# Kernel optimization log

Hardware: AMD Instinct MI355X
Metric: run time of the kernel (lower is better)

## Reference

```python
import jax, jax.numpy as jnp
import numpy as np

B, NL, NP = 8, 256, 16384
DL, DP = 10, 4          # ligand / protein atom-type vocab sizes (one-hot prefix)
L_BIND, L_MREG = 1.0, 0.1
DELTA, EPS, A_C, B_C = 0.01, 1.0, 1.0, 1.0
BOX = 30.0              # Angstrom box for coordinates


def setup_inputs() -> dict:
    key = jax.random.key(0)
    ks = jax.random.split(key, 10)
    return {
        "predicted_noise": jax.random.normal(ks[0], (B, NL, 3), jnp.float32),
        "target_coords": jax.random.normal(ks[1], (B, NL, 3), jnp.float32),
        "scaffold_coords": jax.random.normal(ks[2], (B, NL, 3), jnp.float32),
        "target_coords2": jax.random.uniform(ks[3], (B, NL, 3), jnp.float32) * BOX,
        "target_features": jax.random.uniform(ks[4], (B, NL, DL), jnp.float32),
        "mask": jax.random.uniform(ks[5], (B, NL), jnp.float32),
        "protein_coords": jax.random.uniform(ks[6], (B, NP, 3), jnp.float32) * BOX,
        "protein_features": jax.random.uniform(ks[7], (B, NP, DP), jnp.float32),
        "lig_charge_table": jax.random.normal(ks[8], (DL,), jnp.float32) * 0.3,
        "prot_charge_table": jax.random.normal(ks[9], (DP,), jnp.float32) * 0.3,
    }


def _cdist(x, p):
    # x: [B, NL, 3], p: [B, NP, 3] -> [B, NL, NP] Euclidean distances
    x2 = jnp.sum(x * x, axis=-1)
    p2 = jnp.sum(p * p, axis=-1)
    d2 = x2[:, :, None] + p2[:, None, :] - 2.0 * jnp.einsum('bnd,bmd->bnm', x, p)
    return jnp.sqrt(jnp.maximum(d2, 0.0))


def _binding_energy(x0, prot, lig_feat, prot_feat, lig_tab, prot_tab):
    # atom charges from one-hot prefix of features (argmax lookup)
    ql = lig_tab[jnp.argmax(lig_feat[..., :DL], axis=-1)]    # [B, NL]
    qp = prot_tab[jnp.argmax(prot_feat[..., :DP], axis=-1)]  # [B, NP]
    d = _cdist(x0, prot) + DELTA                             # [B, NL, NP]
    inv = 1.0 / d
    inv6 = inv ** 6
    elec = jnp.sum(ql[:, :, None] * qp[:, None, :] * inv / EPS, axis=(1, 2))
    vdw = jnp.sum(A_C * inv6 * inv6 - B_C * inv6, axis=(1, 2))
    return elec + vdw  # [B]


def reference(predicted_noise, target_coords, scaffold_coords, target_coords2,
              target_features, mask, protein_coords, protein_features,
              lig_charge_table, prot_charge_table):
    msum = jnp.sum(mask)
    # masked denoising MSE
    mse = (predicted_noise - target_coords) ** 2
    loss_denoise = jnp.sum(mse * mask[..., None]) / msum
    # protein-guided binding energy, mean over batch
    loss_bind = jnp.mean(_binding_energy(target_coords2, protein_coords,
                                         target_features, protein_features,
                                         lig_charge_table, prot_charge_table))
    # mask regularization
    mask_diff = jnp.sum((scaffold_coords - target_coords) ** 2, axis=-1)
    loss_mreg = jnp.sum(mask_diff * mask) / msum
    return loss_denoise + L_BIND * loss_bind + L_MREG * loss_mreg
```

## Files before the change

### kernel.cpp

```cpp
#include <hip/hip_runtime.h>
#include <math.h>

#define B   8
#define NL  256
#define NP  16384
#define DL  10
#define DP  4

#define DELTA  0.01f

static __device__ __forceinline__ float fast_sqrtf(float x) {
#if __has_builtin(__builtin_amdgcn_sqrtf)
    return __builtin_amdgcn_sqrtf(x);
#else
    return sqrtf(x);
#endif
}
static __device__ __forceinline__ float fast_rcpf(float x) {
#if __has_builtin(__builtin_amdgcn_rcpf)
    return __builtin_amdgcn_rcpf(x);
#else
    return 1.0f / x;
#endif
}

#define NBIND 2048
#define NMSE  8

__global__ __launch_bounds__(256) void pair_mse_kernel(
    const float* __restrict__ prot_coords,
    const float* __restrict__ prot_feat,
    const float* __restrict__ tc2,
    const float* __restrict__ lig_feat,
    const float* __restrict__ lig_tab,
    const float* __restrict__ prot_tab,
    const float* __restrict__ pred_noise,
    const float* __restrict__ tgt_coords,
    const float* __restrict__ scaf_coords,
    const float* __restrict__ mask,
    double* __restrict__ partials)
{
    const int tid = threadIdx.x;
    const int blk = blockIdx.x;

    if (blk < NBIND) {
        const int lchunk = blk & 3;
        const int pchunk = (blk >> 2) & 63;
        const int b      = blk >> 8;

        __shared__ float4 slig[64];
        if (tid < 64) {
            const int li = b * NL + lchunk * 64 + tid;
            const float* f = lig_feat + (size_t)li * DL;
            float best = f[0]; float q = lig_tab[0];
            #pragma unroll
            for (int j = 1; j < DL; ++j) {
                float v = f[j];
                float t = lig_tab[j];
                if (v > best) { best = v; q = t; }
            }
            const float* c = tc2 + (size_t)li * 3;
            slig[tid] = make_float4(c[0], c[1], c[2], q);
        }

        const int m = b * NP + pchunk * 256 + tid;
        const float* pc = prot_coords + (size_t)m * 3;
        const float px = pc[0], py = pc[1], pz = pc[2];
        const float4 pf = reinterpret_cast<const float4*>(prot_feat)[m];
        float qb = pf.x, qp = prot_tab[0];
        { float t = prot_tab[1]; if (pf.y > qb) { qb = pf.y; qp = t; } }
        { float t = prot_tab[2]; if (pf.z > qb) { qb = pf.z; qp = t; } }
        { float t = prot_tab[3]; if (pf.w > qb) { qb = pf.w; qp = t; } }

        __syncthreads();

        float eacc = 0.0f, vacc = 0.0f;
        #pragma unroll 8
        for (int j = 0; j < 64; ++j) {
            const float4 l = slig[j];
            float dx = l.x - px;
            float dy = l.y - py;
            float dz = l.z - pz;
            float d2 = fmaf(dx, dx, fmaf(dy, dy, dz * dz));
            float d  = fast_sqrtf(d2) + DELTA;
            float inv  = fast_rcpf(d);
            float inv2 = inv * inv;
            float inv6 = inv2 * inv2 * inv2;
            eacc = fmaf(l.w, inv, eacc);
            vacc = fmaf(inv6, inv6 - 1.0f, vacc);
        }
        double e = (double)(qp * eacc);
        double v = (double)vacc;

        #pragma unroll
        for (int off = 32; off > 0; off >>= 1) {
            e += __shfl_down(e, off, 64);
            v += __shfl_down(v, off, 64);
        }
        __shared__ double se[4], sv[4];
        const int lane = tid & 63, w = tid >> 6;
        if (lane == 0) { se[w] = e; sv[w] = v; }
        __syncthreads();
        if (tid == 0) {
            partials[2 * blk]     = se[0] + se[1] + se[2] + se[3];
            partials[2 * blk + 1] = sv[0] + sv[1] + sv[2] + sv[3];
        }
    } else {
        const int idx = blk - NBIND;
        const int i   = idx * 256 + tid;
        float mk = mask[i];
        float a0 = pred_noise[3*i+0] - tgt_coords[3*i+0];
        float a1 = pred_noise[3*i+1] - tgt_coords[3*i+1];
        float a2 = pred_noise[3*i+2] - tgt_coords[3*i+2];
        double de = (double)mk * ((double)a0*a0 + (double)a1*a1 + (double)a2*a2);
        float s0 = scaf_coords[3*i+0] - tgt_coords[3*i+0];
        float s1 = scaf_coords[3*i+1] - tgt_coords[3*i+1];
        float s2 = scaf_coords[3*i+2] - tgt_coords[3*i+2];
        double mr = (double)mk * ((double)s0*s0 + (double)s1*s1 + (double)s2*s2);
        double ms = (double)mk;

        #pragma unroll
        for (int off = 32; off > 0; off >>= 1) {
            de += __shfl_down(de, off, 64);
            mr += __shfl_down(mr, off, 64);
            ms += __shfl_down(ms, off, 64);
        }
        __shared__ double s[4][3];
        const int lane = tid & 63, w = tid >> 6;
        if (lane == 0) { s[w][0] = de; s[w][1] = mr; s[w][2] = ms; }
        __syncthreads();
        if (tid == 0) {
            partials[2*NBIND + idx*3 + 0] = s[0][0]+s[1][0]+s[2][0]+s[3][0];
            partials[2*NBIND + idx*3 + 1] = s[0][1]+s[1][1]+s[2][1]+s[3][1];
            partials[2*NBIND + idx*3 + 2] = s[0][2]+s[1][2]+s[2][2]+s[3][2];
        }
    }
}

__global__ __launch_bounds__(256) void finalize_kernel(
    const double* __restrict__ partials,
    float* __restrict__ out)
{
    const int tid = threadIdx.x;
    double el = 0.0, vd = 0.0;
    for (int i = tid; i < NBIND; i += 256) {
        el += partials[2*i];
        vd += partials[2*i + 1];
    }
    double de = 0.0, mr = 0.0, ms = 0.0;
    if (tid < NMSE) {
        de = partials[2*NBIND + tid*3 + 0];
        mr = partials[2*NBIND + tid*3 + 1];
        ms = partials[2*NBIND + tid*3 + 2];
    }
    #pragma unroll
    for (int off = 32; off > 0; off >>= 1) {
        el += __shfl_down(el, off, 64);
        vd += __shfl_down(vd, off, 64);
        de += __shfl_down(de, off, 64);
        mr += __shfl_down(mr, off, 64);
        ms += __shfl_down(ms, off, 64);
    }
    __shared__ double s[4][5];
    const int lane = tid & 63, w = tid >> 6;
    if (lane == 0) { s[w][0]=el; s[w][1]=vd; s[w][2]=de; s[w][3]=mr; s[w][4]=ms; }
    __syncthreads();
    if (tid == 0) {
        el = s[0][0]+s[1][0]+s[2][0]+s[3][0];
        vd = s[0][1]+s[1][1]+s[2][1]+s[3][1];
        de = s[0][2]+s[1][2]+s[2][2]+s[3][2];
        mr = s[0][3]+s[1][3]+s[2][3]+s[3][3];
        ms = s[0][4]+s[1][4]+s[2][4]+s[3][4];
        double loss_bind = (el + vd) / (double)B;
        double loss = de / ms + loss_bind + 0.1 * (mr / ms);
        out[0] = (float)loss;
    }
}

extern "C" void kernel_launch(void* const* d_in, const int* in_sizes, int n_in,
                              void* d_out, int out_size, void* d_ws, size_t ws_size,
                              hipStream_t stream)
{
    const float* pred_noise  = (const float*)d_in[0];
    const float* tgt_coords  = (const float*)d_in[1];
    const float* scaf_coords = (const float*)d_in[2];
    const float* tc2         = (const float*)d_in[3];
    const float* lig_feat    = (const float*)d_in[4];
    const float* mask        = (const float*)d_in[5];
    const float* prot_coords = (const float*)d_in[6];
    const float* prot_feat   = (const float*)d_in[7];
    const float* lig_tab     = (const float*)d_in[8];
    const float* prot_tab    = (const float*)d_in[9];
    float* out = (float*)d_out;

    double* partials = (double*)d_ws;

    pair_mse_kernel<<<NBIND + NMSE, 256, 0, stream>>>(
        prot_coords, prot_feat, tc2, lig_feat, lig_tab, prot_tab,
        pred_noise, tgt_coords, scaf_coords, mask, partials);
    finalize_kernel<<<1, 256, 0, stream>>>(partials, out);
}
```

Baseline: 94.97 us.

## Fuse finalize into main kernel via last-block atomic counter and pack pair math

Removes the separate finalize kernel launch. Each block bumps an atomic counter after writing its partials, and the last block to arrive does the final reduction and writes the loss. A memset of the counter is added before the launch. The inner pair loop is also restructured to handle two ligand atoms at once using float2 vectors from SoA shared arrays, aiming for packed FP32 math. The risks are the added memset operation and relying on correct memory ordering between blocks.

```diff
diff --git a/kernel.cpp b/kernel.cpp
--- a/kernel.cpp
+++ b/kernel.cpp
@@ -8,6 +8,12 @@
 #define DP  4
 
 #define DELTA  0.01f
+
+#define NBIND 2048
+#define NMSE  8
+#define NBLK  (NBIND + NMSE)
+
+typedef float v2f __attribute__((ext_vector_type(2)));
 
 static __device__ __forceinline__ float fast_sqrtf(float x) {
 #if __has_builtin(__builtin_amdgcn_sqrtf)
@@ -24,10 +30,7 @@
 #endif
 }
 
-#define NBIND 2048
-#define NMSE  8
-
-__global__ __launch_bounds__(256) void pair_mse_kernel(
+__global__ __launch_bounds__(256) void fused_kernel(
     const float* __restrict__ prot_coords,
     const float* __restrict__ prot_feat,
     const float* __restrict__ tc2,
@@ -38,17 +41,22 @@
     const float* __restrict__ tgt_coords,
     const float* __restrict__ scaf_coords,
     const float* __restrict__ mask,
-    double* __restrict__ partials)
+    unsigned*    __restrict__ counter,
+    double*      __restrict__ partials,
+    float*       __restrict__ out)
 {
     const int tid = threadIdx.x;
     const int blk = blockIdx.x;
+    const int lane = tid & 63, w = tid >> 6;
+
+    __shared__ double sred[4][3];
 
     if (blk < NBIND) {
         const int lchunk = blk & 3;
         const int pchunk = (blk >> 2) & 63;
         const int b      = blk >> 8;
 
-        __shared__ float4 slig[64];
+        __shared__ float sx[64], sy[64], sz[64], sw[64];
         if (tid < 64) {
             const int li = b * NL + lchunk * 64 + tid;
             const float* f = lig_feat + (size_t)li * DL;
@@ -60,7 +68,7 @@
                 if (v > best) { best = v; q = t; }
             }
             const float* c = tc2 + (size_t)li * 3;
-            slig[tid] = make_float4(c[0], c[1], c[2], q);
+            sx[tid] = c[0]; sy[tid] = c[1]; sz[tid] = c[2]; sw[tid] = q;
         }
 
         const int m = b * NP + pchunk * 256 + tid;
@@ -74,36 +82,45 @@
 
         __syncthreads();
 
-        float eacc = 0.0f, vacc = 0.0f;
+        v2f eacc = {0.0f, 0.0f}, vacc = {0.0f, 0.0f};
         #pragma unroll 8
-        for (int j = 0; j < 64; ++j) {
-            const float4 l = slig[j];
-            float dx = l.x - px;
-            float dy = l.y - py;
-            float dz = l.z - pz;
-            float d2 = fmaf(dx, dx, fmaf(dy, dy, dz * dz));
-            float d  = fast_sqrtf(d2) + DELTA;
-            float inv  = fast_rcpf(d);
-            float inv2 = inv * inv;
-            float inv6 = inv2 * inv2 * inv2;
-            eacc = fmaf(l.w, inv, eacc);
-            vacc = fmaf(inv6, inv6 - 1.0f, vacc);
-        }
-        double e = (double)(qp * eacc);
-        double v = (double)vacc;
-
+        for (int j = 0; j < 64; j += 2) {
+            v2f lx = *(const v2f*)&sx[j];
+            v2f ly = *(const v2f*)&sy[j];
+            v2f lz = *(const v2f*)&sz[j];
+            v2f lw = *(const v2f*)&sw[j];
+            v2f dx = lx - px;
+            v2f dy = ly - py;
+            v2f dz = lz - pz;
+            v2f d2 = __builtin_elementwise_fma(dx, dx,
+                     __builtin_elementwise_fma(dy, dy, dz * dz));
+            v2f d;
+            d.x = fast_sqrtf(d2.x);
+            d.y = fast_sqrtf(d2.y);
+            d += DELTA;
+            v2f inv;
+            inv.x = fast_rcpf(d.x);
+            inv.y = fast_rcpf(d.y);
+            v2f inv2 = inv * inv;
+            v2f inv6 = inv2 * inv2 * inv2;
+            eacc = __builtin_elementwise_fma(lw, inv, eacc);
+            vacc = __builtin_elementwise_fma(inv6, inv6 - 1.0f, vacc);
+        }
+
+        double e = (double)(qp * (eacc.x + eacc.y));
+        double v = (double)(vacc.x + vacc.y);
         #pragma unroll
         for (int off = 32; off > 0; off >>= 1) {
             e += __shfl_down(e, off, 64);
             v += __shfl_down(v, off, 64);
         }
-        __shared__ double se[4], sv[4];
-        const int lane = tid & 63, w = tid >> 6;
-        if (lane == 0) { se[w] = e; sv[w] = v; }
+        if (lane == 0) { sred[w][0] = e; sred[w][1] = v; }
         __syncthreads();
         if (tid == 0) {
-            partials[2 * blk]     = se[0] + se[1] + se[2] + se[3];
-            partials[2 * blk + 1] = sv[0] + sv[1] + sv[2] + sv[3];
+            double pe = sred[0][0] + sred[1][0] + sred[2][0] + sred[3][0];
+            double pv = sred[0][1] + sred[1][1] + sred[2][1] + sred[3][1];
+            __hip_atomic_store(&partials[2*blk],   pe, __ATOMIC_RELAXED, __HIP_MEMORY_SCOPE_AGENT);
+            __hip_atomic_store(&partials[2*blk+1], pv, __ATOMIC_RELAXED, __HIP_MEMORY_SCOPE_AGENT);
         }
     } else {
         const int idx = blk - NBIND;
@@ -118,62 +135,62 @@
         float s2 = scaf_coords[3*i+2] - tgt_coords[3*i+2];
         double mr = (double)mk * ((double)s0*s0 + (double)s1*s1 + (double)s2*s2);
         double ms = (double)mk;
-
         #pragma unroll
         for (int off = 32; off > 0; off >>= 1) {
             de += __shfl_down(de, off, 64);
             mr += __shfl_down(mr, off, 64);
             ms += __shfl_down(ms, off, 64);
         }
-        __shared__ double s[4][3];
-        const int lane = tid & 63, w = tid >> 6;
-        if (lane == 0) { s[w][0] = de; s[w][1] = mr; s[w][2] = ms; }
+        if (lane == 0) { sred[w][0] = de; sred[w][1] = mr; sred[w][2] = ms; }
         __syncthreads();
         if (tid == 0) {
-            partials[2*NBIND + idx*3 + 0] = s[0][0]+s[1][0]+s[2][0]+s[3][0];
-            partials[2*NBIND + idx*3 + 1] = s[0][1]+s[1][1]+s[2][1]+s[3][1];
-            partials[2*NBIND + idx*3 + 2] = s[0][2]+s[1][2]+s[2][2]+s[3][2];
+            double pd = sred[0][0] + sred[1][0] + sred[2][0] + sred[3][0];
+            double pm = sred[0][1] + sred[1][1] + sred[2][1] + sred[3][1];
+            double pq = sred[0][2] + sred[1][2] + sred[2][2] + sred[3][2];
+            __hip_atomic_store(&partials[2*NBIND + idx*3 + 0], pd, __ATOMIC_RELAXED, __HIP_MEMORY_SCOPE_AGENT);
+            __hip_atomic_store(&partials[2*NBIND + idx*3 + 1], pm, __ATOMIC_RELAXED, __HIP_MEMORY_SCOPE_AGENT);
+            __hip_atomic_store(&partials[2*NBIND + idx*3 + 2], pq, __ATOMIC_RELAXED, __HIP_MEMORY_SCOPE_AGENT);
         }
     }
-}
-
-__global__ __launch_bounds__(256) void finalize_kernel(
-    const double* __restrict__ partials,
-    float* __restrict__ out)
-{
-    const int tid = threadIdx.x;
-    double el = 0.0, vd = 0.0;
-    for (int i = tid; i < NBIND; i += 256) {
-        el += partials[2*i];
-        vd += partials[2*i + 1];
+
+    __shared__ unsigned sOld;
+    if (tid == 0) {
+        sOld = __hip_atomic_fetch_add(counter, 1u, __ATOMIC_ACQ_REL, __HIP_MEMORY_SCOPE_AGENT);
     }
-    double de = 0.0, mr = 0.0, ms = 0.0;
-    if (tid < NMSE) {
-        de = partials[2*NBIND + tid*3 + 0];
-        mr = partials[2*NBIND + tid*3 + 1];
-        ms = partials[2*NBIND + tid*3 + 2];
-    }
-    #pragma unroll
-    for (int off = 32; off > 0; off >>= 1) {
-        el += __shfl_down(el, off, 64);
-        vd += __shfl_down(vd, off, 64);
-        de += __shfl_down(de, off, 64);
-        mr += __shfl_down(mr, off, 64);
-        ms += __shfl_down(ms, off, 64);
-    }
-    __shared__ double s[4][5];
-    const int lane = tid & 63, w = tid >> 6;
-    if (lane == 0) { s[w][0]=el; s[w][1]=vd; s[w][2]=de; s[w][3]=mr; s[w][4]=ms; }
     __syncthreads();
-    if (tid == 0) {
-        el = s[0][0]+s[1][0]+s[2][0]+s[3][0];
-        vd = s[0][1]+s[1][1]+s[2][1]+s[3][1];
-        de = s[0][2]+s[1][2]+s[2][2]+s[3][2];
-        mr = s[0][3]+s[1][3]+s[2][3]+s[3][3];
-        ms = s[0][4]+s[1][4]+s[2][4]+s[3][4];
-        double loss_bind = (el + vd) / (double)B;
-        double loss = de / ms + loss_bind + 0.1 * (mr / ms);
-        out[0] = (float)loss;
+    if (sOld == NBLK - 1) {
+        double el = 0.0, vd = 0.0;
+        for (int i = tid; i < NBIND; i += 256) {
+            el += __hip_atomic_load(&partials[2*i],   __ATOMIC_RELAXED, __HIP_MEMORY_SCOPE_AGENT);
+            vd += __hip_atomic_load(&partials[2*i+1], __ATOMIC_RELAXED, __HIP_MEMORY_SCOPE_AGENT);
+        }
+        double de = 0.0, mr = 0.0, ms = 0.0;
+        if (tid < NMSE) {
+            de = __hip_atomic_load(&partials[2*NBIND + tid*3 + 0], __ATOMIC_RELAXED, __HIP_MEMORY_SCOPE_AGENT);
+            mr = __hip_atomic_load(&partials[2*NBIND + tid*3 + 1], __ATOMIC_RELAXED, __HIP_MEMORY_SCOPE_AGENT);
+            ms = __hip_atomic_load(&partials[2*NBIND + tid*3 + 2], __ATOMIC_RELAXED, __HIP_MEMORY_SCOPE_AGENT);
+        }
+        #pragma unroll
+        for (int off = 32; off > 0; off >>= 1) {
+            el += __shfl_down(el, off, 64);
+            vd += __shfl_down(vd, off, 64);
+            de += __shfl_down(de, off, 64);
+            mr += __shfl_down(mr, off, 64);
+            ms += __shfl_down(ms, off, 64);
+        }
+        __shared__ double sf[4][5];
+        if (lane == 0) { sf[w][0]=el; sf[w][1]=vd; sf[w][2]=de; sf[w][3]=mr; sf[w][4]=ms; }
+        __syncthreads();
+        if (tid == 0) {
+            el = sf[0][0]+sf[1][0]+sf[2][0]+sf[3][0];
+            vd = sf[0][1]+sf[1][1]+sf[2][1]+sf[3][1];
+            de = sf[0][2]+sf[1][2]+sf[2][2]+sf[3][2];
+            mr = sf[0][3]+sf[1][3]+sf[2][3]+sf[3][3];
+            ms = sf[0][4]+sf[1][4]+sf[2][4]+sf[3][4];
+            double loss_bind = (el + vd) / (double)B;
+            double loss = de / ms + loss_bind + 0.1 * (mr / ms);
+            out[0] = (float)loss;
+        }
     }
 }
 
@@ -193,10 +210,11 @@
     const float* prot_tab    = (const float*)d_in[9];
     float* out = (float*)d_out;
 
-    double* partials = (double*)d_ws;
-
-    pair_mse_kernel<<<NBIND + NMSE, 256, 0, stream>>>(
+    unsigned* counter = (unsigned*)d_ws;
+    double*   partials = (double*)((char*)d_ws + 16);
+
+    hipMemsetAsync(counter, 0, sizeof(unsigned), stream);
+    fused_kernel<<<NBLK, 256, 0, stream>>>(
         prot_coords, prot_feat, tc2, lig_feat, lig_tab, prot_tab,
-        pred_noise, tgt_coords, scaf_coords, mask, partials);
-    finalize_kernel<<<1, 256, 0, stream>>>(partials, out);
-}
+        pred_noise, tgt_coords, scaf_coords, mask, counter, partials, out);
+}
```

Result: slower. 120.0 us (+26.4%).

## Double ligand tile per block, stage via coalesced SMEM loads, vectorize pair loop

Applied to the files above, without the earlier changes.

Each block now processes 128 ligand atoms instead of 64, which halves the block count and reuses the protein atom loaded into registers across twice as many pairs. Ligand coordinates and features are first copied into shared memory with coalesced loads, and the argmax charge lookup then runs from shared memory into a structure-of-arrays layout. The inner loop reads 4 ligand atoms at once as vector loads and keeps 4-wide accumulators. The trade-off is an extra __syncthreads, more shared memory per block and fewer blocks to spread across the CUs.

```diff
diff --git a/kernel.cpp b/kernel.cpp
--- a/kernel.cpp
+++ b/kernel.cpp
@@ -8,6 +8,12 @@
 #define DP  4
 
 #define DELTA  0.01f
+
+#define NBINDBLK 1024
+#define NMSE     8
+#define LATOMS   128
+
+typedef float v4f __attribute__((ext_vector_type(4)));
 
 static __device__ __forceinline__ float fast_sqrtf(float x) {
 #if __has_builtin(__builtin_amdgcn_sqrtf)
@@ -23,9 +29,6 @@
     return 1.0f / x;
 #endif
 }
-
-#define NBIND 2048
-#define NMSE  8
 
 __global__ __launch_bounds__(256) void pair_mse_kernel(
     const float* __restrict__ prot_coords,
@@ -38,29 +41,32 @@
     const float* __restrict__ tgt_coords,
     const float* __restrict__ scaf_coords,
     const float* __restrict__ mask,
-    double* __restrict__ partials)
+    double*      __restrict__ partials)
 {
-    const int tid = threadIdx.x;
-    const int blk = blockIdx.x;
-
-    if (blk < NBIND) {
-        const int lchunk = blk & 3;
-        const int pchunk = (blk >> 2) & 63;
-        const int b      = blk >> 8;
-
-        __shared__ float4 slig[64];
-        if (tid < 64) {
-            const int li = b * NL + lchunk * 64 + tid;
-            const float* f = lig_feat + (size_t)li * DL;
-            float best = f[0]; float q = lig_tab[0];
+    const int tid  = threadIdx.x;
+    const int blk  = blockIdx.x;
+    const int lane = tid & 63, w = tid >> 6;
+
+    __shared__ double sred[4][3];
+
+    if (blk < NBINDBLK) {
+        const int lhalf  = blk & 1;
+        const int pchunk = (blk >> 1) & 63;
+        const int b      = blk >> 7;
+
+        __shared__ __align__(16) float sx[LATOMS], sy[LATOMS], sz[LATOMS], sw[LATOMS];
+        __shared__ float sc[LATOMS * 3];
+        __shared__ float sfeat[LATOMS * DL];
+
+        const int abase = b * NL + lhalf * LATOMS;
+
+        {
+            const float* csrc = tc2 + (size_t)abase * 3;
             #pragma unroll
-            for (int j = 1; j < DL; ++j) {
-                float v = f[j];
-                float t = lig_tab[j];
-                if (v > best) { best = v; q = t; }
-            }
-            const float* c = tc2 + (size_t)li * 3;
-            slig[tid] = make_float4(c[0], c[1], c[2], q);
+            for (int t = tid; t < LATOMS * 3; t += 256) sc[t] = csrc[t];
+            const float* fsrc = lig_feat + (size_t)abase * DL;
+            #pragma unroll
+            for (int t = tid; t < LATOMS * DL; t += 256) sfeat[t] = fsrc[t];
         }
 
         const int m = b * NP + pchunk * 256 + tid;
@@ -74,39 +80,62 @@
 
         __syncthreads();
 
-        float eacc = 0.0f, vacc = 0.0f;
-        #pragma unroll 8
-        for (int j = 0; j < 64; ++j) {
-            const float4 l = slig[j];
-            float dx = l.x - px;
-            float dy = l.y - py;
-            float dz = l.z - pz;
-            float d2 = fmaf(dx, dx, fmaf(dy, dy, dz * dz));
-            float d  = fast_sqrtf(d2) + DELTA;
-            float inv  = fast_rcpf(d);
-            float inv2 = inv * inv;
-            float inv6 = inv2 * inv2 * inv2;
-            eacc = fmaf(l.w, inv, eacc);
-            vacc = fmaf(inv6, inv6 - 1.0f, vacc);
-        }
-        double e = (double)(qp * eacc);
-        double v = (double)vacc;
-
+        if (tid < LATOMS) {
+            float best = sfeat[tid * DL];
+            float q = lig_tab[0];
+            #pragma unroll
+            for (int j = 1; j < DL; ++j) {
+                float v = sfeat[tid * DL + j];
+                float t = lig_tab[j];
+                if (v > best) { best = v; q = t; }
+            }
+            sx[tid] = sc[tid * 3 + 0];
+            sy[tid] = sc[tid * 3 + 1];
+            sz[tid] = sc[tid * 3 + 2];
+            sw[tid] = q;
+        }
+        __syncthreads();
+
+        v4f eacc = {0.f, 0.f, 0.f, 0.f}, vacc = {0.f, 0.f, 0.f, 0.f};
+        #pragma unroll 4
+        for (int j = 0; j < LATOMS; j += 4) {
+            v4f lx = *(const v4f*)&sx[j];
+            v4f ly = *(const v4f*)&sy[j];
+            v4f lz = *(const v4f*)&sz[j];
+            v4f lw = *(const v4f*)&sw[j];
+            v4f dx = lx - px;
+            v4f dy = ly - py;
+            v4f dz = lz - pz;
+            v4f d2 = __builtin_elementwise_fma(dx, dx,
+                     __builtin_elementwise_fma(dy, dy, dz * dz));
+            v4f d;
+            d.x = fast_sqrtf(d2.x); d.y = fast_sqrtf(d2.y);
+            d.z = fast_sqrtf(d2.z); d.w = fast_sqrtf(d2.w);
+            d += DELTA;
+            v4f inv;
+            inv.x = fast_rcpf(d.x); inv.y = fast_rcpf(d.y);
+            inv.z = fast_rcpf(d.z); inv.w = fast_rcpf(d.w);
+            v4f inv2 = inv * inv;
+            v4f inv6 = inv2 * inv2 * inv2;
+            eacc = __builtin_elementwise_fma(lw, inv, eacc);
+            vacc = __builtin_elementwise_fma(inv6, inv6 - 1.0f, vacc);
+        }
+
+        double e = (double)(qp * ((eacc.x + eacc.y) + (eacc.z + eacc.w)));
+        double v = (double)((vacc.x + vacc.y) + (vacc.z + vacc.w));
         #pragma unroll
         for (int off = 32; off > 0; off >>= 1) {
             e += __shfl_down(e, off, 64);
             v += __shfl_down(v, off, 64);
         }
-        __shared__ double se[4], sv[4];
-        const int lane = tid & 63, w = tid >> 6;
-        if (lane == 0) { se[w] = e; sv[w] = v; }
+        if (lane == 0) { sred[w][0] = e; sred[w][1] = v; }
         __syncthreads();
         if (tid == 0) {
-            partials[2 * blk]     = se[0] + se[1] + se[2] + se[3];
-            partials[2 * blk + 1] = sv[0] + sv[1] + sv[2] + sv[3];
+            partials[2 * blk]     = sred[0][0] + sred[1][0] + sred[2][0] + sred[3][0];
+            partials[2 * blk + 1] = sred[0][1] + sred[1][1] + sred[2][1] + sred[3][1];
         }
     } else {
-        const int idx = blk - NBIND;
+        const int idx = blk - NBINDBLK;
         const int i   = idx * 256 + tid;
         float mk = mask[i];
         float a0 = pred_noise[3*i+0] - tgt_coords[3*i+0];
@@ -118,21 +147,18 @@
         float s2 = scaf_coords[3*i+2] - tgt_coords[3*i+2];
         double mr = (double)mk * ((double)s0*s0 + (double)s1*s1 + (double)s2*s2);
         double ms = (double)mk;
-
         #pragma unroll
         for (int off = 32; off > 0; off >>= 1) {
             de += __shfl_down(de, off, 64);
             mr += __shfl_down(mr, off, 64);
             ms += __shfl_down(ms, off, 64);
         }
-        __shared__ double s[4][3];
-        const int lane = tid & 63, w = tid >> 6;
-        if (lane == 0) { s[w][0] = de; s[w][1] = mr; s[w][2] = ms; }
+        if (lane == 0) { sred[w][0] = de; sred[w][1] = mr; sred[w][2] = ms; }
         __syncthreads();
         if (tid == 0) {
-            partials[2*NBIND + idx*3 + 0] = s[0][0]+s[1][0]+s[2][0]+s[3][0];
-            partials[2*NBIND + idx*3 + 1] = s[0][1]+s[1][1]+s[2][1]+s[3][1];
-            partials[2*NBIND + idx*3 + 2] = s[0][2]+s[1][2]+s[2][2]+s[3][2];
+            partials[2*NBINDBLK + idx*3 + 0] = sred[0][0]+sred[1][0]+sred[2][0]+sred[3][0];
+            partials[2*NBINDBLK + idx*3 + 1] = sred[0][1]+sred[1][1]+sred[2][1]+sred[3][1];
+            partials[2*NBINDBLK + idx*3 + 2] = sred[0][2]+sred[1][2]+sred[2][2]+sred[3][2];
         }
     }
 }
@@ -142,16 +168,17 @@
     float* __restrict__ out)
 {
     const int tid = threadIdx.x;
+    const int lane = tid & 63, w = tid >> 6;
     double el = 0.0, vd = 0.0;
-    for (int i = tid; i < NBIND; i += 256) {
+    for (int i = tid; i < NBINDBLK; i += 256) {
         el += partials[2*i];
         vd += partials[2*i + 1];
     }
     double de = 0.0, mr = 0.0, ms = 0.0;
     if (tid < NMSE) {
-        de = partials[2*NBIND + tid*3 + 0];
-        mr = partials[2*NBIND + tid*3 + 1];
-        ms = partials[2*NBIND + tid*3 + 2];
+        de = partials[2*NBINDBLK + tid*3 + 0];
+        mr = partials[2*NBINDBLK + tid*3 + 1];
+        ms = partials[2*NBINDBLK + tid*3 + 2];
     }
     #pragma unroll
     for (int off = 32; off > 0; off >>= 1) {
@@ -162,7 +189,6 @@
         ms += __shfl_down(ms, off, 64);
     }
     __shared__ double s[4][5];
-    const int lane = tid & 63, w = tid >> 6;
     if (lane == 0) { s[w][0]=el; s[w][1]=vd; s[w][2]=de; s[w][3]=mr; s[w][4]=ms; }
     __syncthreads();
     if (tid == 0) {
@@ -195,7 +221,7 @@
 
     double* partials = (double*)d_ws;
 
-    pair_mse_kernel<<<NBIND + NMSE, 256, 0, stream>>>(
+    pair_mse_kernel<<<NBINDBLK + NMSE, 256, 0, stream>>>(
         prot_coords, prot_feat, tc2, lig_feat, lig_tab, prot_tab,
         pred_noise, tgt_coords, scaf_coords, mask, partials);
     finalize_kernel<<<1, 256, 0, stream>>>(partials, out);
```

Measured after the change: 91.41 us. 3.8% less time.
